# Kernel tuning notes

Hardware: AMD Instinct MI355X
Metric: run time of the kernel (lower is better)

## Reference

```python
import jax, jax.numpy as jnp
import numpy as np

T_TOK, N_NODES, N_EDGES, D_FEAT, D_PE, SPD_LEN, BATCH = 10, 4096, 65536, 128, 32, 4, 64


def setup_inputs() -> dict:
    key = jax.random.key(0)
    ks = jax.random.split(key, 8)
    B, N, E, T, D, PE, L = BATCH, N_NODES, N_EDGES, T_TOK, D_FEAT, D_PE, SPD_LEN
    return {
        "g_x": jax.random.normal(ks[0], (B, N, D), jnp.float32),
        "g_pe": jax.random.normal(ks[1], (B, N, PE), jnp.float32),
        "g_edge_index": jax.random.randint(ks[2], (B, 2, E), 0, N),
        "g_spd": jax.random.randint(ks[3], (B, N), 0, 8),  # some values exceed L to exercise clamp
        "g_root": jax.random.randint(ks[4], (B,), 0, N),
        "token_list": jax.random.normal(ks[5], (T, D), jnp.float32) * 0.1,
        "token_pe": jnp.zeros((T, PE), jnp.float32),
        "shared_edge_weight": jnp.asarray(1.0, jnp.float32),
        "edge_weight_param": jnp.ones((L + 1,), jnp.float32),
    }


def _static_indices(T, N):
    # inner prompt-token edges: complete graph minus self loops, row-major (dense_to_sparse order)
    ii, jj = np.meshgrid(np.arange(T), np.arange(T), indexing='ij')
    m = ii != jj
    inner = np.stack([ii[m], jj[m]])            # [2, T*(T-1)]
    # cross edges: meshgrid(token, node) row-major, node ids offset by T
    src = np.repeat(np.arange(T), N)
    dst = np.tile(np.arange(N), T) + T
    fwd = np.stack([src, dst])                  # [2, T*N]
    cross = np.concatenate([fwd, fwd[::-1]], axis=1)  # to_undirected: both directions, [2, 2*T*N]
    return jnp.asarray(inner), jnp.asarray(cross)


def reference(g_x, g_pe, g_edge_index, g_spd, g_root,
              token_list, token_pe, shared_edge_weight, edge_weight_param):
    B, N, D = g_x.shape
    T = token_list.shape[0]
    E = g_edge_index.shape[2]
    L = edge_weight_param.shape[0] - 1
    inner, cross = _static_indices(T, N)
    Ei, Ec = inner.shape[1], cross.shape[1]

    # per-graph node-id offset (Batch.from_data_list concatenation)
    off = (jnp.arange(B, dtype=g_edge_index.dtype) * (T + N))[:, None, None]
    edge_index = jnp.concatenate([
        jnp.broadcast_to(inner[None].astype(g_edge_index.dtype), (B, 2, Ei)),
        g_edge_index + T,
        jnp.broadcast_to(cross[None].astype(g_edge_index.dtype), (B, 2, Ec)),
    ], axis=2) + off                                  # [B, 2, Etot]
    edge_index = edge_index.transpose(1, 0, 2).reshape(2, -1)

    # cross edge weights: edge_weight_param[clamp(spd)] per destination node, tiled over tokens,
    # duplicated for the reversed direction (to_undirected reduce='mean' over unique pairs)
    w_node = edge_weight_param[jnp.clip(g_spd, 0, L)]          # [B, N]
    cw = jnp.tile(w_node, (1, T))                              # [B, T*N]
    edge_weight = jnp.concatenate([
        jnp.broadcast_to(shared_edge_weight, (B, Ei)),         # inner prompt edges
        jnp.ones((B, E), g_x.dtype),                           # original graph edges
        cw, cw,                                                # undirected cross edges
    ], axis=1).reshape(-1)

    x = jnp.concatenate([jnp.broadcast_to(token_list[None], (B, T, D)), g_x], axis=1).reshape(-1, D)
    pe = jnp.concatenate([jnp.broadcast_to(token_pe[None], (B, T, token_pe.shape[1])), g_pe], axis=1)
    pe = pe.reshape(-1, token_pe.shape[1])
    root = g_root + T + jnp.arange(B, dtype=g_root.dtype) * (T + N)
    return x, pe, edge_index, edge_weight, root
```

## Files before the change

kernel.cpp:

```cpp
#include <hip/hip_runtime.h>

#define T_TOK 10
#define NN    4096
#define NE    65536
#define DF    128
#define DPE   32
#define LSPD  4
#define BB    64

#define TN    (T_TOK + NN)
#define EI    (T_TOK * (T_TOK - 1))
#define EC    (2 * T_TOK * NN)
#define ETOT  (EI + NE + EC)
#define BE    (BB * ETOT)

#define SX ((long long)BB * TN * DF)
#define SP ((long long)BB * TN * DPE)
#define SE (2LL * BE)
#define SW ((long long)BE)

__global__ __launch_bounds__(256) void k_fill_x(
    const float4* __restrict__ gx, const float4* __restrict__ tok,
    float4* __restrict__ ox, int total)
{
    const int R4 = DF / 4;
    for (int i = blockIdx.x * blockDim.x + threadIdx.x; i < total;
         i += gridDim.x * blockDim.x) {
        int row = i >> 5;
        int c   = i & 31;
        int b   = row / TN;
        int lr  = row - b * TN;
        float4 v;
        if (lr < T_TOK) v = tok[lr * R4 + c];
        else            v = gx[(b * NN + (lr - T_TOK)) * R4 + c];
        ox[i] = v;
    }
}

__global__ __launch_bounds__(256) void k_fill_pe(
    const float4* __restrict__ gpe, const float4* __restrict__ tokpe,
    float4* __restrict__ ope, int total)
{
    const int R4 = DPE / 4;
    for (int i = blockIdx.x * blockDim.x + threadIdx.x; i < total;
         i += gridDim.x * blockDim.x) {
        int row = i >> 3;
        int c   = i & 7;
        int b   = row / TN;
        int lr  = row - b * TN;
        float4 v;
        if (lr < T_TOK) v = tokpe[lr * R4 + c];
        else            v = gpe[(b * NN + (lr - T_TOK)) * R4 + c];
        ope[i] = v;
    }
}

__global__ __launch_bounds__(256) void k_edges(
    const int* __restrict__ gei, const int* __restrict__ spd,
    const float* __restrict__ ewp, const float* __restrict__ swp,
    float* __restrict__ oei, float* __restrict__ oew)
{
    for (int i = blockIdx.x * blockDim.x + threadIdx.x; i < BE;
         i += gridDim.x * blockDim.x) {
        int b = i / ETOT;
        int e = i - b * ETOT;
        int base = b * TN;
        int s, d;
        float w;
        if (e < EI) {
            int ii = e / (T_TOK - 1);
            int k  = e - ii * (T_TOK - 1);
            int jj = k + (k >= ii ? 1 : 0);
            s = ii; d = jj;
            w = swp[0];
        } else if (e < EI + NE) {
            int ge = e - EI;
            s = gei[(2 * b + 0) * NE + ge] + T_TOK;
            d = gei[(2 * b + 1) * NE + ge] + T_TOK;
            w = 1.0f;
        } else {
            int c = e - EI - NE;
            int n;
            if (c < T_TOK * NN) {
                int t = c >> 12;
                n = c & (NN - 1);
                s = t; d = n + T_TOK;
            } else {
                int c2 = c - T_TOK * NN;
                int t = c2 >> 12;
                n = c2 & (NN - 1);
                s = n + T_TOK; d = t;
            }
            int sv = spd[b * NN + n];
            sv = min(max(sv, 0), LSPD);
            w = ewp[sv];
        }
        s += base; d += base;
        oei[i]            = (float)s;
        oei[(long long)BE + i] = (float)d;
        oew[i] = w;
    }
}

__global__ __launch_bounds__(64) void k_root(
    const int* __restrict__ groot, float* __restrict__ oroot)
{
    int b = threadIdx.x;
    if (b < BB) oroot[b] = (float)(groot[b] + T_TOK + b * TN);
}

extern "C" void kernel_launch(void* const* d_in, const int* in_sizes, int n_in,
                              void* d_out, int out_size, void* d_ws, size_t ws_size,
                              hipStream_t stream) {
    const float* g_x       = (const float*)d_in[0];
    const float* g_pe      = (const float*)d_in[1];
    const int*   g_ei      = (const int*)d_in[2];
    const int*   g_spd     = (const int*)d_in[3];
    const int*   g_root    = (const int*)d_in[4];
    const float* token     = (const float*)d_in[5];
    const float* token_pe  = (const float*)d_in[6];
    const float* shared_w  = (const float*)d_in[7];
    const float* ew_param  = (const float*)d_in[8];

    float* out    = (float*)d_out;
    float* out_x  = out;
    float* out_pe = out + SX;
    float* out_ei = out + SX + SP;
    float* out_ew = out + SX + SP + SE;
    float* out_rt = out + SX + SP + SE + SW;

    {
        int total = (int)(SX / 4);
        int blocks = (total + 255) / 256;
        k_fill_x<<<blocks, 256, 0, stream>>>(
            (const float4*)g_x, (const float4*)token, (float4*)out_x, total);
    }
    {
        int total = (int)(SP / 4);
        int blocks = (total + 255) / 256;
        k_fill_pe<<<blocks, 256, 0, stream>>>(
            (const float4*)g_pe, (const float4*)token_pe, (float4*)out_pe, total);
    }
    {
        int blocks = (BE + 255) / 256;
        k_edges<<<blocks, 256, 0, stream>>>(
            g_ei, g_spd, ew_param, shared_w, out_ei, out_ew);
    }
    k_root<<<1, 64, 0, stream>>>(g_root, out_rt);
}
```

Baseline: 429.1 us.

## Fuse all fills into one persistent kernel with nontemporal vector accesses

Merges the four launches (x copy, pe copy, edge generation, root) into a single grid-stride kernel with a fixed grid of 2048 blocks covering a unified index space. The edge section now handles two edges per thread with 8-byte vector loads and stores. All bulk copies use nontemporal loads and stores to avoid polluting cache. This is meant to remove launch overhead and tail gaps between kernels and to widen edge-section accesses. The cost is per-iteration branching and an int-sized index space where overflow must be checked.

```diff
diff --git a/kernel.cpp b/kernel.cpp
--- a/kernel.cpp
+++ b/kernel.cpp
@@ -14,137 +14,116 @@
 #define ETOT  (EI + NE + EC)
 #define BE    (BB * ETOT)
 
-#define SX ((long long)BB * TN * DF)
-#define SP ((long long)BB * TN * DPE)
-#define SE (2LL * BE)
-#define SW ((long long)BE)
+#define SX (BB * TN * DF)
+#define SP (BB * TN * DPE)
+#define SE (2 * BE)
+#define SW (BE)
 
-__global__ __launch_bounds__(256) void k_fill_x(
-    const float4* __restrict__ gx, const float4* __restrict__ tok,
-    float4* __restrict__ ox, int total)
+#define UX (SX / 4)
+#define UP (SP / 4)
+#define UE (BE / 2)
+#define PEB (ETOT / 2)
+#define UTOT (UX + UP + UE + BB)
+
+typedef float f32x4 __attribute__((ext_vector_type(4)));
+typedef float f32x2 __attribute__((ext_vector_type(2)));
+typedef int   i32x2 __attribute__((ext_vector_type(2)));
+
+__global__ __launch_bounds__(256) void k_all(
+    const f32x4* __restrict__ gx, const f32x4* __restrict__ gpe,
+    const int* __restrict__ gei, const int* __restrict__ spd,
+    const int* __restrict__ groot,
+    const f32x4* __restrict__ tok, const f32x4* __restrict__ tokpe,
+    const float* __restrict__ swp, const float* __restrict__ ewp,
+    float* __restrict__ out)
 {
-    const int R4 = DF / 4;
-    for (int i = blockIdx.x * blockDim.x + threadIdx.x; i < total;
-         i += gridDim.x * blockDim.x) {
-        int row = i >> 5;
-        int c   = i & 31;
-        int b   = row / TN;
-        int lr  = row - b * TN;
-        float4 v;
-        if (lr < T_TOK) v = tok[lr * R4 + c];
-        else            v = gx[(b * NN + (lr - T_TOK)) * R4 + c];
-        ox[i] = v;
+    const int stride = gridDim.x * blockDim.x;
+    for (int u = blockIdx.x * blockDim.x + threadIdx.x; u < UTOT; u += stride) {
+        if (u < UX) {
+            int row = u >> 5, c = u & 31;
+            int b = row / TN, lr = row - b * TN;
+            f32x4 v;
+            if (lr < T_TOK) v = tok[lr * 32 + c];
+            else            v = __builtin_nontemporal_load(&gx[(b * NN + lr - T_TOK) * 32 + c]);
+            __builtin_nontemporal_store(v, &((f32x4*)out)[u]);
+        } else if (u < UX + UP) {
+            int q = u - UX;
+            int row = q >> 3, c = q & 7;
+            int b = row / TN, lr = row - b * TN;
+            f32x4 v;
+            if (lr < T_TOK) v = tokpe[lr * 8 + c];
+            else            v = __builtin_nontemporal_load(&gpe[(b * NN + lr - T_TOK) * 8 + c]);
+            __builtin_nontemporal_store(v, &((f32x4*)out)[u]);
+        } else if (u < UX + UP + UE) {
+            int p  = u - (UX + UP);
+            int b  = p / PEB;
+            int e0 = 2 * (p - b * PEB);
+            int base = b * TN;
+            f32x2 s2, d2, w2;
+            if (e0 < EI) {
+                int e1 = e0 + 1;
+                int i0 = e0 / (T_TOK - 1), k0 = e0 - i0 * (T_TOK - 1);
+                int i1 = e1 / (T_TOK - 1), k1 = e1 - i1 * (T_TOK - 1);
+                int j0 = k0 + (k0 >= i0 ? 1 : 0);
+                int j1 = k1 + (k1 >= i1 ? 1 : 0);
+                float w = swp[0];
+                s2 = (f32x2){(float)(i0 + base), (float)(i1 + base)};
+                d2 = (f32x2){(float)(j0 + base), (float)(j1 + base)};
+                w2 = (f32x2){w, w};
+            } else if (e0 < EI + NE) {
+                int ge = e0 - EI;
+                i32x2 sa = __builtin_nontemporal_load((const i32x2*)&gei[(2 * b + 0) * NE + ge]);
+                i32x2 da = __builtin_nontemporal_load((const i32x2*)&gei[(2 * b + 1) * NE + ge]);
+                s2 = (f32x2){(float)(sa.x + T_TOK + base), (float)(sa.y + T_TOK + base)};
+                d2 = (f32x2){(float)(da.x + T_TOK + base), (float)(da.y + T_TOK + base)};
+                w2 = (f32x2){1.0f, 1.0f};
+            } else {
+                int c = e0 - EI - NE;
+                int n, s0, d0, s1, d1;
+                if (c < T_TOK * NN) {
+                    int t = c >> 12; n = c & (NN - 1);
+                    s0 = t;          d0 = n + T_TOK;
+                    s1 = t;          d1 = n + 1 + T_TOK;
+                } else {
+                    int c2 = c - T_TOK * NN;
+                    int t = c2 >> 12; n = c2 & (NN - 1);
+                    s0 = n + T_TOK;     d0 = t;
+                    s1 = n + 1 + T_TOK; d1 = t;
+                }
+                i32x2 sv = *(const i32x2*)&spd[b * NN + n];
+                int v0 = min(max(sv.x, 0), LSPD);
+                int v1 = min(max(sv.y, 0), LSPD);
+                w2 = (f32x2){ewp[v0], ewp[v1]};
+                s2 = (f32x2){(float)(s0 + base), (float)(s1 + base)};
+                d2 = (f32x2){(float)(d0 + base), (float)(d1 + base)};
+            }
+            int i0 = b * ETOT + e0;
+            float* oei = out + (SX + SP);
+            float* oew = out + (SX + SP + SE);
+            __builtin_nontemporal_store(s2, (f32x2*)&oei[i0]);
+            __builtin_nontemporal_store(d2, (f32x2*)&oei[BE + i0]);
+            __builtin_nontemporal_store(w2, (f32x2*)&oew[i0]);
+        } else {
+            int b = u - (UX + UP + UE);
+            out[SX + SP + SE + SW + b] = (float)(groot[b] + T_TOK + b * TN);
+        }
     }
-}
-
-__global__ __launch_bounds__(256) void k_fill_pe(
-    const float4* __restrict__ gpe, const float4* __restrict__ tokpe,
-    float4* __restrict__ ope, int total)
-{
-    const int R4 = DPE / 4;
-    for (int i = blockIdx.x * blockDim.x + threadIdx.x; i < total;
-         i += gridDim.x * blockDim.x) {
-        int row = i >> 3;
-        int c   = i & 7;
-        int b   = row / TN;
-        int lr  = row - b * TN;
-        float4 v;
-        if (lr < T_TOK) v = tokpe[lr * R4 + c];
-        else            v = gpe[(b * NN + (lr - T_TOK)) * R4 + c];
-        ope[i] = v;
-    }
-}
-
-__global__ __launch_bounds__(256) void k_edges(
-    const int* __restrict__ gei, const int* __restrict__ spd,
-    const float* __restrict__ ewp, const float* __restrict__ swp,
-    float* __restrict__ oei, float* __restrict__ oew)
-{
-    for (int i = blockIdx.x * blockDim.x + threadIdx.x; i < BE;
-         i += gridDim.x * blockDim.x) {
-        int b = i / ETOT;
-        int e = i - b * ETOT;
-        int base = b * TN;
-        int s, d;
-        float w;
-        if (e < EI) {
-            int ii = e / (T_TOK - 1);
-            int k  = e - ii * (T_TOK - 1);
-            int jj = k + (k >= ii ? 1 : 0);
-            s = ii; d = jj;
-            w = swp[0];
-        } else if (e < EI + NE) {
-            int ge = e - EI;
-            s = gei[(2 * b + 0) * NE + ge] + T_TOK;
-            d = gei[(2 * b + 1) * NE + ge] + T_TOK;
-            w = 1.0f;
-        } else {
-            int c = e - EI - NE;
-            int n;
-            if (c < T_TOK * NN) {
-                int t = c >> 12;
-                n = c & (NN - 1);
-                s = t; d = n + T_TOK;
-            } else {
-                int c2 = c - T_TOK * NN;
-                int t = c2 >> 12;
-                n = c2 & (NN - 1);
-                s = n + T_TOK; d = t;
-            }
-            int sv = spd[b * NN + n];
-            sv = min(max(sv, 0), LSPD);
-            w = ewp[sv];
-        }
-        s += base; d += base;
-        oei[i]            = (float)s;
-        oei[(long long)BE + i] = (float)d;
-        oew[i] = w;
-    }
-}
-
-__global__ __launch_bounds__(64) void k_root(
-    const int* __restrict__ groot, float* __restrict__ oroot)
-{
-    int b = threadIdx.x;
-    if (b < BB) oroot[b] = (float)(groot[b] + T_TOK + b * TN);
 }
 
 extern "C" void kernel_launch(void* const* d_in, const int* in_sizes, int n_in,
                               void* d_out, int out_size, void* d_ws, size_t ws_size,
                               hipStream_t stream) {
-    const float* g_x       = (const float*)d_in[0];
-    const float* g_pe      = (const float*)d_in[1];
-    const int*   g_ei      = (const int*)d_in[2];
-    const int*   g_spd     = (const int*)d_in[3];
-    const int*   g_root    = (const int*)d_in[4];
-    const float* token     = (const float*)d_in[5];
-    const float* token_pe  = (const float*)d_in[6];
-    const float* shared_w  = (const float*)d_in[7];
-    const float* ew_param  = (const float*)d_in[8];
+    const f32x4* g_x      = (const f32x4*)d_in[0];
+    const f32x4* g_pe     = (const f32x4*)d_in[1];
+    const int*   g_ei     = (const int*)d_in[2];
+    const int*   g_spd    = (const int*)d_in[3];
+    const int*   g_root   = (const int*)d_in[4];
+    const f32x4* token    = (const f32x4*)d_in[5];
+    const f32x4* token_pe = (const f32x4*)d_in[6];
+    const float* shared_w = (const float*)d_in[7];
+    const float* ew_param = (const float*)d_in[8];
 
-    float* out    = (float*)d_out;
-    float* out_x  = out;
-    float* out_pe = out + SX;
-    float* out_ei = out + SX + SP;
-    float* out_ew = out + SX + SP + SE;
-    float* out_rt = out + SX + SP + SE + SW;
-
-    {
-        int total = (int)(SX / 4);
-        int blocks = (total + 255) / 256;
-        k_fill_x<<<blocks, 256, 0, stream>>>(
-            (const float4*)g_x, (const float4*)token, (float4*)out_x, total);
-    }
-    {
-        int total = (int)(SP / 4);
-        int blocks = (total + 255) / 256;
-        k_fill_pe<<<blocks, 256, 0, stream>>>(
-            (const float4*)g_pe, (const float4*)token_pe, (float4*)out_pe, total);
-    }
-    {
-        int blocks = (BE + 255) / 256;
-        k_edges<<<blocks, 256, 0, stream>>>(
-            g_ei, g_spd, ew_param, shared_w, out_ei, out_ew);
-    }
-    k_root<<<1, 64, 0, stream>>>(g_root, out_rt);
+    k_all<<<2048, 256, 0, stream>>>(g_x, g_pe, g_ei, g_spd, g_root,
+                                    token, token_pe, shared_w, ew_param,
+                                    (float*)d_out);
 }
```

Result: no change. 430.9 us (+0.4%).
